# Kernel tuning notes

Measured on AMD Instinct MI355X. Metric: run time of the kernel, lower is better.

## Reference

```python
import jax, jax.numpy as jnp
import numpy as np


def _cas(N):
    # Hartley cas matrix: cos(2*pi*k*n/N) + sin(2*pi*k*n/N), shape [N, N]
    n = jnp.arange(N, dtype=jnp.float32)
    ang = 2.0 * jnp.pi * n[:, None] * n[None, :] / N
    return jnp.cos(ang) + jnp.sin(ang)


def setup_inputs() -> dict:
    key = jax.random.key(0)
    k0, k1, k2, k3, k4 = jax.random.split(key, 5)
    B, N, C = 8, 4096, 768
    nb, bs, hf = 8, 96, 1
    scale = 0.02
    return {
        "x": jax.random.normal(k0, (B, N, C), jnp.float32),
        "w1": scale * jax.random.normal(k1, (2, nb, bs, bs * hf), jnp.float32),
        "b1": scale * jax.random.normal(k2, (2, nb, bs * hf), jnp.float32),
        "w2": scale * jax.random.normal(k3, (2, nb, bs * hf, bs), jnp.float32),
        "b2": scale * jax.random.normal(k4, (2, nb, bs), jnp.float32),
    }


def reference(x, w1, b1, w2, b2):
    SPARSITY = 0.01       # sparsity_threshold (softshrink lambda)
    FRAC = 1.0            # hard_thresholding_fraction
    B, N, C = x.shape
    H = W = int(np.sqrt(N))
    nb, bs = w1.shape[1], w1.shape[2]
    bias = x

    xf = x.astype(jnp.float32).reshape(B, H, W, C)
    cas = _cas(C)  # module's dht2d transforms the LAST (channel) dim
    xr = xf @ cas  # [B,H,W,C]; imag part is exactly zero after torch.complex(x, 0)
    xr = xr.reshape(B, H, W, nb, bs)

    # kept_modes = int((N//2+1)*frac), clamped by W-dim slicing semantics
    km = min(W, int((N // 2 + 1) * FRAC))

    # block-diagonal 2-layer MLP on (real, imag) with imag input == 0
    o1r = jax.nn.relu(jnp.einsum('bhwki,kio->bhwko', xr, w1[0]) + b1[0])
    o1i = jax.nn.relu(jnp.einsum('bhwki,kio->bhwko', xr, w1[1]) + b1[1])
    o2r = (jnp.einsum('bhwko,koc->bhwkc', o1r, w2[0])
           - jnp.einsum('bhwko,koc->bhwkc', o1i, w2[1]) + b2[0])
    o2i = (jnp.einsum('bhwko,koc->bhwkc', o1i, w2[0])
           + jnp.einsum('bhwko,koc->bhwkc', o1r, w2[1]) + b2[1])

    if km < W:
        mask = (jnp.arange(W) < km)[None, None, :, None, None]
        o2r = jnp.where(mask, o2r, 0.0)
        o2i = jnp.where(mask, o2i, 0.0)

    # softshrink on stacked real/imag
    ss = lambda v: jnp.sign(v) * jnp.maximum(jnp.abs(v) - SPARSITY, 0.0)
    o2r, o2i = ss(o2r), ss(o2i)

    real = o2r.reshape(B, H, W, C)
    imag = o2i.reshape(B, H, W, C)

    # idht2d: dht2d(complex) = real@cas - imag@cas, divided by TOTAL element count
    n_tot = B * H * W * C
    out = ((real - imag) @ cas) / n_tot
    out = out.reshape(B, N, C).astype(bias.dtype)
    return out + bias
```

## Files before the change

kernel.cpp:

```cpp
#include <hip/hip_runtime.h>
#include <hip/hip_bf16.h>
#include <cstdint>
#include <cstddef>

typedef __bf16 bf8_t __attribute__((ext_vector_type(8)));
typedef __bf16 bf4_t __attribute__((ext_vector_type(4)));
typedef float  f4_t  __attribute__((ext_vector_type(4)));

#define CC 768
#define NROWS 32768
#define NTOT 25165824

__device__ __forceinline__ void gld16(const void* g, void* l) {
  __builtin_amdgcn_global_load_lds(
      (const __attribute__((address_space(1))) void*)g,
      (__attribute__((address_space(3))) void*)l, 16, 0, 0);
}


__global__ void make_cas(__bf16* __restrict__ cas) {
  int idx = blockIdx.x * 256 + threadIdx.x;
  int i = idx / CC, j = idx - i * CC;
  int ij = (i * j) % CC;
  float ang = 6.283185307179586f * (float)ij / (float)CC;
  cas[idx] = (__bf16)(__cosf(ang) + __sinf(ang));
}

__global__ void cvt4(const float* __restrict__ x, __bf16* __restrict__ o) {
  int i = (blockIdx.x * 256 + threadIdx.x) * 4;
  float4 v = *(const float4*)(x + i);
  bf4_t r;
  r[0] = (__bf16)v.x; r[1] = (__bf16)v.y; r[2] = (__bf16)v.z; r[3] = (__bf16)v.w;
  *(bf4_t*)(o + i) = r;
}

__global__ void pack_w1(const float* __restrict__ w1, __bf16* __restrict__ w1f) {
  int f = blockIdx.x * 256 + threadIdx.x;
  int j = f & 7, lane = (f >> 3) & 63, rest = f >> 9;
  int nt = rest % 12, kt = (rest / 12) % 3, blk = rest / 36;
  int k = kt * 32 + (lane >> 4) * 8 + j;
  int o = nt * 16 + (lane & 15);
  float v = (o < 96) ? w1[(0 * 8 + blk) * 9216 + k * 96 + o]
                     : w1[(1 * 8 + blk) * 9216 + k * 96 + (o - 96)];
  w1f[f] = (__bf16)v;
}

__global__ void pack_w2(const float* __restrict__ w2, __bf16* __restrict__ w2f) {
  int f = blockIdx.x * 256 + threadIdx.x;
  int j = f & 7, lane = (f >> 3) & 63, rest = f >> 9;
  int nt = rest % 12, kt = (rest / 12) % 6, blk = rest / 72;
  int i = kt * 32 + (lane >> 4) * 8 + j;
  int o = nt * 16 + (lane & 15);
  float v;
  if (o < 96) v = (i < 96) ?  w2[(0 * 8 + blk) * 9216 + i * 96 + o]
                           : -w2[(1 * 8 + blk) * 9216 + (i - 96) * 96 + o];
  else        v = (i < 96) ?  w2[(1 * 8 + blk) * 9216 + i * 96 + (o - 96)]
                           :  w2[(0 * 8 + blk) * 9216 + (i - 96) * 96 + (o - 96)];
  w2f[f] = (__bf16)v;
}

__global__ __launch_bounds__(256, 2) void gemm_back(
    const __bf16* __restrict__ Zb, const __bf16* __restrict__ BT,
    float* __restrict__ Cf, const float* __restrict__ Xres, float scale)
{
  __shared__ __align__(16) char smem[49152];
  const int t = threadIdx.x;
  const int lane = t & 63, wid = t >> 6;
  const int wm = (wid >> 1) * 64, wn = (wid & 1) * 64;

  const int id = blockIdx.x;
  const int sid = (id & 7) * 192 + (id >> 3);
  const int m0 = (sid / 6) * 128, n0 = (sid % 6) * 128;

  const int q = lane >> 4, r = lane & 15;
  const __bf16* gA = Zb + (size_t)(m0 + (t >> 2)) * CC + (t & 3) * 8;
  const __bf16* gB = BT + (size_t)(n0 + (t >> 2)) * CC + (t & 3) * 8;
  const int ldsOff = (t >> 2) * 32 + (t & 3) * 8;

  auto stage = [&](int b, int tile) {
    int k0 = tile * 32;
    __bf16* lA = (__bf16*)(smem + b * 16384) + ldsOff;
    __bf16* lB = (__bf16*)(smem + b * 16384 + 8192) + ldsOff;
    gld16(gA + k0, lA);
    gld16(gA + (size_t)64 * CC + k0, lA + 64 * 32);
    gld16(gB + k0, lB);
    gld16(gB + (size_t)64 * CC + k0, lB + 64 * 32);
  };

  f4_t acc[4][4] = {};
  stage(0, 0);
  stage(1, 1);
  for (int tile = 0; tile < 24; ++tile) {
    int nt = tile + 2; if (nt > 23) nt = 23;
    stage((tile + 2) % 3, nt);
    asm volatile("s_waitcnt vmcnt(8)" ::: "memory");
    __builtin_amdgcn_s_barrier();
    const __bf16* sA = (const __bf16*)(smem + (tile % 3) * 16384);
    const __bf16* sB = sA + 8192 / 2;
    bf8_t af[4], bfr[4];
#pragma unroll
    for (int i = 0; i < 4; i++)
      af[i] = *(const bf8_t*)(sA + (wm + i * 16 + r) * 32 + q * 8);
#pragma unroll
    for (int j = 0; j < 4; j++)
      bfr[j] = *(const bf8_t*)(sB + (wn + j * 16 + r) * 32 + q * 8);
#pragma unroll
    for (int i = 0; i < 4; i++)
#pragma unroll
      for (int j = 0; j < 4; j++)
        acc[i][j] = __builtin_amdgcn_mfma_f32_16x16x32_bf16(af[i], bfr[j], acc[i][j], 0, 0, 0);
    __builtin_amdgcn_s_barrier();
  }

  float* cs = (float*)smem;
#pragma unroll
  for (int h = 0; h < 2; ++h) {
    __builtin_amdgcn_s_barrier();
    if ((wid >> 1) == h) {
#pragma unroll
      for (int i = 0; i < 4; i++)
#pragma unroll
        for (int j = 0; j < 4; j++)
#pragma unroll
          for (int rr = 0; rr < 4; rr++)
            cs[(i * 16 + q * 4 + rr) * 132 + wn + j * 16 + r] = acc[i][j][rr];
    }
    __builtin_amdgcn_s_barrier();
    const int u = t & 31, row8 = t >> 5;
#pragma unroll
    for (int p = 0; p < 8; ++p) {
      int rl = p * 8 + row8;
      size_t goff = (size_t)(m0 + h * 64 + rl) * CC + n0 + u * 4;
      f4_t xr = *(const f4_t*)(Xres + goff);
      f4_t cv = *(const f4_t*)(cs + rl * 132 + u * 4);
      f4_t o;
      o[0] = cv[0] * scale + xr[0];
      o[1] = cv[1] * scale + xr[1];
      o[2] = cv[2] * scale + xr[2];
      o[3] = cv[3] * scale + xr[3];
      *(f4_t*)(Cf + goff) = o;
    }
  }
}

__global__ __launch_bounds__(384, 3) void fused3(
    const __bf16* __restrict__ A, const __bf16* __restrict__ BT,
    const __bf16* __restrict__ w1f, const __bf16* __restrict__ w2f,
    const float* __restrict__ b1, const float* __restrict__ b2,
    __bf16* __restrict__ Z)
{
  __shared__ __align__(16) char smem[63488];
  __bf16* Hs = (__bf16*)smem;
  __bf16* vt = (__bf16*)(smem + 25600);
  __bf16* zl = (__bf16*)(smem + 51200);

  const int t = threadIdx.x, lane = t & 63, w = t >> 6;
  const int id = blockIdx.x;
  const int sid = (id & 7) * 128 + (id >> 3);
  const int cbp = sid & 3;
  const int m0 = (sid >> 2) * 128;
  const int n0 = cbp * 192;
  const int q = lane >> 4, r = lane & 15;

  const __bf16* gA  = A  + (size_t)(m0 + (t >> 2)) * CC + (t & 3) * 8;
  const __bf16* gA2 = A  + (size_t)(m0 + 96 + (t >> 2)) * CC + (t & 3) * 8;
  const __bf16* gB  = BT + (size_t)(n0 + (t >> 2)) * CC + (t & 3) * 8;
  const __bf16* gB2 = BT + (size_t)(n0 + 96 + (t >> 2)) * CC + (t & 3) * 8;

  auto stage = [&](int b, int tile) {
    int k0 = tile * 32;
    char* base = smem + b * 20480;
    gld16(gA + k0, (__bf16*)base + t * 8);
    if (t < 128) gld16(gA2 + k0, (__bf16*)base + (384 + t) * 8);
    gld16(gB + k0, (__bf16*)(base + 8192) + t * 8);
    gld16(gB2 + k0, (__bf16*)(base + 8192) + (384 + t) * 8);
  };

  f4_t acc[8][2] = {};
  stage(0, 0);
  stage(1, 1);
  for (int tile = 0; tile < 24; ++tile) {
    int nt = tile + 2; if (nt > 23) nt = 23;
    stage((tile + 2) % 3, nt);
    if (w < 2) asm volatile("s_waitcnt vmcnt(8)" ::: "memory");
    else       asm volatile("s_waitcnt vmcnt(6)" ::: "memory");
    __builtin_amdgcn_s_barrier();
    const __bf16* sA = (const __bf16*)(smem + (tile % 3) * 20480);
    const __bf16* sB = (const __bf16*)(smem + (tile % 3) * 20480 + 8192);
    bf8_t af[8], bfr[2];
#pragma unroll
    for (int i = 0; i < 8; i++)
      af[i] = *(const bf8_t*)(sA + (i * 16 + r) * 32 + q * 8);
#pragma unroll
    for (int j = 0; j < 2; j++)
      bfr[j] = *(const bf8_t*)(sB + (w * 32 + j * 16 + r) * 32 + q * 8);
#pragma unroll
    for (int i = 0; i < 8; i++)
#pragma unroll
      for (int j = 0; j < 2; j++)
        acc[i][j] = __builtin_amdgcn_mfma_f32_16x16x32_bf16(af[i], bfr[j], acc[i][j], 0, 0, 0);
    __builtin_amdgcn_s_barrier();
  }
  asm volatile("s_waitcnt vmcnt(0)" ::: "memory");
  __builtin_amdgcn_s_barrier();

#pragma unroll
  for (int h = 0; h < 2; h++) {
#pragma unroll
    for (int ii = 0; ii < 4; ii++)
#pragma unroll
      for (int j = 0; j < 2; j++) {
        int col = w * 32 + j * 16 + r;
#pragma unroll
        for (int rr = 0; rr < 4; rr++) {
          int row = ii * 16 + q * 4 + rr;
          vt[row * 200 + col] = (__bf16)acc[h * 4 + ii][j][rr];
        }
      }
    __syncthreads();

#pragma unroll
    for (int cb = 0; cb < 2; cb++) {
      const int bidx = cbp * 2 + cb;
      const __bf16* w1b = w1f + (size_t)bidx * (36 * 64 * 8);
      const __bf16* w2b = w2f + (size_t)bidx * (72 * 64 * 8);
      bf8_t w1r[3][2], w2r[6][2];
#pragma unroll
      for (int kt = 0; kt < 3; kt++)
#pragma unroll
        for (int j = 0; j < 2; j++)
          w1r[kt][j] = *(const bf8_t*)(w1b + ((size_t)(kt * 12 + 2 * w + j) * 64 + lane) * 8);
#pragma unroll
      for (int kt = 0; kt < 6; kt++) {
        w2r[kt][0] = *(const bf8_t*)(w2b + ((size_t)(kt * 12 + w) * 64 + lane) * 8);
        w2r[kt][1] = *(const bf8_t*)(w2b + ((size_t)(kt * 12 + w + 6) * 64 + lane) * 8);
      }
      float bb[2];
#pragma unroll
      for (int j = 0; j < 2; j++) {
        int c = (2 * w + j) * 16 + r;
        bb[j] = (c < 96) ? b1[bidx * 96 + c] : b1[768 + bidx * 96 + (c - 96)];
      }
      const float br = b2[bidx * 96 + w * 16 + r];
      const float bi = b2[768 + bidx * 96 + w * 16 + r];

#pragma unroll
      for (int rt = 0; rt < 4; rt++) {
        const __bf16* vp = vt + (rt * 16 + r) * 200 + cb * 96 + q * 8;
        f4_t a0 = {}, a1 = {};
#pragma unroll
        for (int kt = 0; kt < 3; kt++) {
          bf8_t a = *(const bf8_t*)(vp + kt * 32);
          a0 = __builtin_amdgcn_mfma_f32_16x16x32_bf16(a, w1r[kt][0], a0, 0, 0, 0);
          a1 = __builtin_amdgcn_mfma_f32_16x16x32_bf16(a, w1r[kt][1], a1, 0, 0, 0);
        }
#pragma unroll
        for (int j = 0; j < 2; j++) {
          int c = (2 * w + j) * 16 + r;
          f4_t* ap = j ? &a1 : &a0;
#pragma unroll
          for (int rr = 0; rr < 4; rr++) {
            float v = (*ap)[rr] + bb[j];
            Hs[(rt * 16 + q * 4 + rr) * 200 + c] = (__bf16)(v > 0.f ? v : 0.f);
          }
        }
      }
      __syncthreads();
#pragma unroll
      for (int rt = 0; rt < 4; rt++) {
        f4_t ar = {}, ai = {};
#pragma unroll
        for (int kt = 0; kt < 6; kt++) {
          bf8_t a = *(const bf8_t*)(&Hs[(rt * 16 + r) * 200 + kt * 32 + q * 8]);
          ar = __builtin_amdgcn_mfma_f32_16x16x32_bf16(a, w2r[kt][0], ar, 0, 0, 0);
          ai = __builtin_amdgcn_mfma_f32_16x16x32_bf16(a, w2r[kt][1], ai, 0, 0, 0);
        }
#pragma unroll
        for (int rr = 0; rr < 4; rr++) {
          float yr = ar[rr] + br, yi = ai[rr] + bi;
          float sr = fabsf(yr) - 0.01f; sr = sr > 0.f ? copysignf(sr, yr) : 0.f;
          float si = fabsf(yi) - 0.01f; si = si > 0.f ? copysignf(si, yi) : 0.f;
          zl[(rt * 16 + q * 4 + rr) * 96 + w * 16 + r] = (__bf16)(sr - si);
        }
      }
      __syncthreads();
      {
        const uint32_t* zsrc = (const uint32_t*)zl;
        int cdw = t % 48, crow = t / 48;
        int rbase = m0 + h * 64;
#pragma unroll
        for (int it = 0; it < 8; it++) {
          int row = it * 8 + crow;
          uint32_t* dst = (uint32_t*)(Z + (size_t)(rbase + row) * CC + n0 + cb * 96);
          dst[cdw] = zsrc[row * 48 + cdw];
        }
      }
    }
  }
}


extern "C" void kernel_launch(void* const* d_in, const int* in_sizes, int n_in,
                              void* d_out, int out_size, void* d_ws, size_t ws_size,
                              hipStream_t stream) {
  const float* x  = (const float*)d_in[0];
  const float* w1 = (const float*)d_in[1];
  const float* b1 = (const float*)d_in[2];
  const float* w2 = (const float*)d_in[3];
  const float* b2 = (const float*)d_in[4];
  float* out = (float*)d_out;

  char* ws = (char*)d_ws;
  size_t off = 0;
  auto alloc = [&](size_t bytes) {
    char* p = ws + off;
    off += (bytes + 255) & ~(size_t)255;
    return p;
  };
  __bf16* casb = (__bf16*)alloc((size_t)CC * CC * 2);
  __bf16* w1f  = (__bf16*)alloc((size_t)8 * 36 * 64 * 8 * 2);
  __bf16* w2f  = (__bf16*)alloc((size_t)8 * 72 * 64 * 8 * 2);
  __bf16* xb   = (__bf16*)alloc((size_t)NTOT * 2);
  __bf16* vv   = (__bf16*)alloc((size_t)NTOT * 2);

  make_cas<<<2304, 256, 0, stream>>>(casb);
  cvt4<<<24576, 256, 0, stream>>>(x, xb);
  pack_w1<<<576, 256, 0, stream>>>(w1, w1f);
  pack_w2<<<1152, 256, 0, stream>>>(w2, w2f);

  fused3<<<1024, 384, 0, stream>>>(xb, casb, w1f, w2f, b1, b2, vv);
  gemm_back<<<1536, 256, 0, stream>>>(vv, casb, out, x, 1.0f / 25165824.0f);
}
```

Baseline: 340.9 us.

## Load GEMM B fragments directly to registers and shrink LDS for higher occupancy

The first GEMM in the fused kernel now streams each wave's cas-matrix fragments from global memory straight into double-buffered registers instead of staging them through LDS. The per-stage LDS buffer shrinks to hold only A. The intermediate vt tile is also written half at a time, one 96-channel block per pass, which cuts the total shared allocation from 63488 to 51200 bytes. Launch bounds rise from 3 to 4 blocks per CU. In exchange, B is read uncoalesced per lane from global or L2, register pressure rises, and an extra __syncthreads is added per channel block.

Result: slower. 504.9 us (+48.1%).

```diff
diff --git a/kernel.cpp b/kernel.cpp
--- a/kernel.cpp
+++ b/kernel.cpp
@@ -143,16 +143,16 @@
   }
 }
 
-__global__ __launch_bounds__(384, 3) void fused3(
+__global__ __launch_bounds__(384, 4) void fused6(
     const __bf16* __restrict__ A, const __bf16* __restrict__ BT,
     const __bf16* __restrict__ w1f, const __bf16* __restrict__ w2f,
     const float* __restrict__ b1, const float* __restrict__ b2,
     __bf16* __restrict__ Z)
 {
-  __shared__ __align__(16) char smem[63488];
+  __shared__ __align__(16) char smem[51200];
   __bf16* Hs = (__bf16*)smem;
   __bf16* vt = (__bf16*)(smem + 25600);
-  __bf16* zl = (__bf16*)(smem + 51200);
+  __bf16* zl = (__bf16*)(smem + 38912);
 
   const int t = threadIdx.x, lane = t & 63, w = t >> 6;
   const int id = blockIdx.x;
@@ -164,63 +164,80 @@
 
   const __bf16* gA  = A  + (size_t)(m0 + (t >> 2)) * CC + (t & 3) * 8;
   const __bf16* gA2 = A  + (size_t)(m0 + 96 + (t >> 2)) * CC + (t & 3) * 8;
-  const __bf16* gB  = BT + (size_t)(n0 + (t >> 2)) * CC + (t & 3) * 8;
-  const __bf16* gB2 = BT + (size_t)(n0 + 96 + (t >> 2)) * CC + (t & 3) * 8;
-
-  auto stage = [&](int b, int tile) {
+  const __bf16* gBf = BT + (size_t)(n0 + w * 32 + r) * CC + q * 8;
+
+  auto stageA = [&](int b, int tile) {
     int k0 = tile * 32;
-    char* base = smem + b * 20480;
+    char* base = smem + b * 8192;
     gld16(gA + k0, (__bf16*)base + t * 8);
     if (t < 128) gld16(gA2 + k0, (__bf16*)base + (384 + t) * 8);
-    gld16(gB + k0, (__bf16*)(base + 8192) + t * 8);
-    gld16(gB2 + k0, (__bf16*)(base + 8192) + (384 + t) * 8);
   };
+  auto loadB = [&](bf8_t* dst, int tile) {
+    int k0 = tile * 32;
+    dst[0] = *(const bf8_t*)(gBf + k0);
+    dst[1] = *(const bf8_t*)(gBf + (size_t)16 * CC + k0);
+  };
 
   f4_t acc[8][2] = {};
-  stage(0, 0);
-  stage(1, 1);
-  for (int tile = 0; tile < 24; ++tile) {
-    int nt = tile + 2; if (nt > 23) nt = 23;
-    stage((tile + 2) % 3, nt);
-    if (w < 2) asm volatile("s_waitcnt vmcnt(8)" ::: "memory");
-    else       asm volatile("s_waitcnt vmcnt(6)" ::: "memory");
-    __builtin_amdgcn_s_barrier();
-    const __bf16* sA = (const __bf16*)(smem + (tile % 3) * 20480);
-    const __bf16* sB = (const __bf16*)(smem + (tile % 3) * 20480 + 8192);
-    bf8_t af[8], bfr[2];
-#pragma unroll
-    for (int i = 0; i < 8; i++)
-      af[i] = *(const bf8_t*)(sA + (i * 16 + r) * 32 + q * 8);
-#pragma unroll
-    for (int j = 0; j < 2; j++)
-      bfr[j] = *(const bf8_t*)(sB + (w * 32 + j * 16 + r) * 32 + q * 8);
-#pragma unroll
-    for (int i = 0; i < 8; i++)
-#pragma unroll
-      for (int j = 0; j < 2; j++)
-        acc[i][j] = __builtin_amdgcn_mfma_f32_16x16x32_bf16(af[i], bfr[j], acc[i][j], 0, 0, 0);
-    __builtin_amdgcn_s_barrier();
-  }
+  bf8_t bP[2], bQ[2];
+  stageA(0, 0);
+  stageA(1, 1);
+  loadB(bP, 0);
+
+#define FUSED6_STEP(TILE, STG_T, BNEXT_T, BDST, BUSE)                          \
+  {                                                                            \
+    stageA(((TILE) + 2) % 3, (STG_T));                                         \
+    loadB((BDST), (BNEXT_T));                                                  \
+    if (w < 2) asm volatile("s_waitcnt vmcnt(4)" ::: "memory");                \
+    else       asm volatile("s_waitcnt vmcnt(3)" ::: "memory");                \
+    __builtin_amdgcn_s_barrier();                                              \
+    const __bf16* sA = (const __bf16*)(smem + ((TILE) % 3) * 8192);            \
+    bf8_t af[8];                                                               \
+    _Pragma("unroll")                                                          \
+    for (int i = 0; i < 8; i++)                                                \
+      af[i] = *(const bf8_t*)(sA + (i * 16 + r) * 32 + q * 8);                 \
+    _Pragma("unroll")                                                          \
+    for (int i = 0; i < 8; i++)                                                \
+      _Pragma("unroll")                                                        \
+      for (int j = 0; j < 2; j++)                                              \
+        acc[i][j] = __builtin_amdgcn_mfma_f32_16x16x32_bf16(af[i], (BUSE)[j],  \
+                                                            acc[i][j], 0, 0, 0);\
+    __builtin_amdgcn_s_barrier();                                              \
+  }
+
+  for (int u = 0; u < 24; u += 2) {
+    int s2 = u + 2; if (s2 > 23) s2 = 23;
+    int s3 = u + 3; if (s3 > 23) s3 = 23;
+    int bn1 = u + 1;
+    int bn2 = u + 2; if (bn2 > 23) bn2 = 23;
+    FUSED6_STEP(u,     s2, bn1, bQ, bP)
+    FUSED6_STEP(u + 1, s3, bn2, bP, bQ)
+  }
+#undef FUSED6_STEP
+
   asm volatile("s_waitcnt vmcnt(0)" ::: "memory");
   __builtin_amdgcn_s_barrier();
 
 #pragma unroll
   for (int h = 0; h < 2; h++) {
 #pragma unroll
-    for (int ii = 0; ii < 4; ii++)
-#pragma unroll
-      for (int j = 0; j < 2; j++) {
-        int col = w * 32 + j * 16 + r;
-#pragma unroll
-        for (int rr = 0; rr < 4; rr++) {
-          int row = ii * 16 + q * 4 + rr;
-          vt[row * 200 + col] = (__bf16)acc[h * 4 + ii][j][rr];
-        }
-      }
-    __syncthreads();
-
-#pragma unroll
     for (int cb = 0; cb < 2; cb++) {
+      if ((w / 3) == cb) {
+        const int wl = w - cb * 3;
+#pragma unroll
+        for (int ii = 0; ii < 4; ii++)
+#pragma unroll
+          for (int j = 0; j < 2; j++) {
+            int col = wl * 32 + j * 16 + r;
+#pragma unroll
+            for (int rr = 0; rr < 4; rr++) {
+              int row = ii * 16 + q * 4 + rr;
+              vt[row * 104 + col] = (__bf16)acc[h * 4 + ii][j][rr];
+            }
+          }
+      }
+      __syncthreads();
+
       const int bidx = cbp * 2 + cb;
       const __bf16* w1b = w1f + (size_t)bidx * (36 * 64 * 8);
       const __bf16* w2b = w2f + (size_t)bidx * (72 * 64 * 8);
@@ -246,7 +263,7 @@
 
 #pragma unroll
       for (int rt = 0; rt < 4; rt++) {
-        const __bf16* vp = vt + (rt * 16 + r) * 200 + cb * 96 + q * 8;
+        const __bf16* vp = vt + (rt * 16 + r) * 104 + q * 8;
         f4_t a0 = {}, a1 = {};
 #pragma unroll
         for (int kt = 0; kt < 3; kt++) {
@@ -328,6 +345,6 @@
   pack_w1<<<576, 256, 0, stream>>>(w1, w1f);
   pack_w2<<<1152, 256, 0, stream>>>(w2, w2f);
 
-  fused3<<<1024, 384, 0, stream>>>(xb, casb, w1f, w2f, b1, b2, vv);
+  fused6<<<1024, 384, 0, stream>>>(xb, casb, w1f, w2f, b1, b2, vv);
   gemm_back<<<1536, 256, 0, stream>>>(vv, casb, out, x, 1.0f / 25165824.0f);
 }
```
